# Kernel tuning notes

Hardware: AMD Instinct MI355X
Metric: run time of the kernel (lower is better)

The kernel has to match this reference:

```python
import jax, jax.numpy as jnp
import numpy as np

INPUT_SIZE = 2
HIDDEN = 128
OUTPUT = 2
FUTURE = 50


def setup_inputs() -> dict:
    key = jax.random.key(0)
    ks = jax.random.split(key, 7)
    B, T = 4096, 512
    s = 1.0 / np.sqrt(HIDDEN)
    x = jax.random.normal(ks[0], (B, T, INPUT_SIZE), dtype=jnp.float32)
    W_ih = jax.random.uniform(ks[1], (4 * HIDDEN, INPUT_SIZE), minval=-s, maxval=s, dtype=jnp.float32)
    W_hh = jax.random.uniform(ks[2], (4 * HIDDEN, HIDDEN), minval=-s, maxval=s, dtype=jnp.float32)
    b_ih = jax.random.uniform(ks[3], (4 * HIDDEN,), minval=-s, maxval=s, dtype=jnp.float32)
    b_hh = jax.random.uniform(ks[4], (4 * HIDDEN,), minval=-s, maxval=s, dtype=jnp.float32)
    fc_w = jax.random.uniform(ks[5], (OUTPUT, HIDDEN), minval=-s, maxval=s, dtype=jnp.float32)
    fc_b = jax.random.uniform(ks[6], (OUTPUT,), minval=-s, maxval=s, dtype=jnp.float32)
    return {"x": x, "W_ih": W_ih, "W_hh": W_hh, "b_ih": b_ih, "b_hh": b_hh, "fc_w": fc_w, "fc_b": fc_b}


def reference(x, W_ih, W_hh, b_ih, b_hh, fc_w, fc_b):
    B = x.shape[0]

    def cell(h, c, xt):
        # gates: [B, 4H], PyTorch LSTMCell order i, f, g, o
        gates = xt @ W_ih.T + b_ih + h @ W_hh.T + b_hh
        i, f, g, o = jnp.split(gates, 4, axis=-1)
        c_new = jax.nn.sigmoid(f) * c + jax.nn.sigmoid(i) * jnp.tanh(g)
        h_new = jax.nn.sigmoid(o) * jnp.tanh(c_new)
        return h_new, c_new

    h0 = jnp.zeros((B, HIDDEN), dtype=x.dtype)
    c0 = jnp.zeros((B, HIDDEN), dtype=x.dtype)

    def encode_step(carry, xt):
        h, c = carry
        h, c = cell(h, c, xt)
        return (h, c), None

    (h, c), _ = jax.lax.scan(encode_step, (h0, c0), jnp.swapaxes(x, 0, 1))

    def forecast_step(carry, _):
        h, c = carry
        y = h @ fc_w.T + fc_b  # [B, OUTPUT]
        h, c = cell(h, c, y)
        return (h, c), y

    (_, _), ys = jax.lax.scan(forecast_step, (h, c), None, length=FUTURE)
    # ys: [FUTURE, B, OUTPUT] -> torch.cat(outputs, dim=1) -> [B, FUTURE*OUTPUT]
    return jnp.swapaxes(ys, 0, 1).reshape(B, FUTURE * OUTPUT)
```

## Files before the change

### kernel.cpp

```cpp
#include <hip/hip_runtime.h>

#define HIDDEN 128
#define TSTEPS 512
#define NFUT 50
#define BR 16
#define THREADS 512
#define HPITCH 136

typedef __bf16 bf16x8 __attribute__((ext_vector_type(8)));
typedef float floatx4 __attribute__((ext_vector_type(4)));

union B8 { int4 i; bf16x8 v; };

#if defined(__has_builtin)
#  if __has_builtin(__builtin_amdgcn_exp2f)
#    define EXP2F(x) __builtin_amdgcn_exp2f(x)
#  else
#    define EXP2F(x) exp2f(x)
#  endif
#  if __has_builtin(__builtin_amdgcn_rcpf)
#    define RCPF(x) __builtin_amdgcn_rcpf(x)
#  else
#    define RCPF(x) (1.0f / (x))
#  endif
#else
#  define EXP2F(x) exp2f(x)
#  define RCPF(x) (1.0f / (x))
#endif

#define L2E  1.4426950408889634f
#define L2E2 2.8853900817779268f

__global__ __launch_bounds__(THREADS, 2)
void lstm_forecast_kernel(const float* __restrict__ x,
                          const float* __restrict__ W_ih,
                          const float* __restrict__ W_hh,
                          const float* __restrict__ b_ih,
                          const float* __restrict__ b_hh,
                          const float* __restrict__ fc_w,
                          const float* __restrict__ fc_b,
                          float* __restrict__ out) {
    __shared__ __align__(16) uint2  xa[(TSTEPS + 1) * BR];
    __shared__ __align__(16) __bf16 h_lds[2][BR * HPITCH];
    __shared__ __align__(16) float  fcw_lds[2][HIDDEN];

    const int tid  = threadIdx.x;
    const int wave = tid >> 6;
    const int lane = tid & 63;
    const int quad = lane >> 4;
    const int l15  = lane & 15;
    const int rb   = blockIdx.x * BR;

    if (tid < 256) fcw_lds[tid >> 7][tid & 127] = fc_w[tid];

    {
        const int row = tid & 15;
        for (int tb = tid >> 4; tb < TSTEPS + 1; tb += THREADS >> 4) {
            float2 xv = make_float2(0.f, 0.f);
            if (tb < TSTEPS)
                xv = *(const float2*)&x[(size_t)(rb + row) * (2 * TSTEPS) + tb * 2];
            __bf16 x0h = (__bf16)xv.x, x1h = (__bf16)xv.y;
            __bf16 x0r = (__bf16)(xv.x - (float)x0h);
            __bf16 x1r = (__bf16)(xv.y - (float)x1h);
            uint2 d;
            d.x = (unsigned)__builtin_bit_cast(unsigned short, x0h) |
                  ((unsigned)__builtin_bit_cast(unsigned short, x1h) << 16);
            d.y = (unsigned)__builtin_bit_cast(unsigned short, x0r) |
                  ((unsigned)__builtin_bit_cast(unsigned short, x1r) << 16);
            xa[tb * BR + row] = d;
        }
    }
    for (int i = tid; i < BR * HPITCH; i += THREADS) h_lds[0][i] = (__bf16)0.0f;

    bf16x8 bfrag[4][4];
    B8 bfx[4];
    float wih0[4], wih1[4], bsum[4], gs[4];
    const int u = wave * 16 + l15;
    const float fcb0 = fc_b[0], fcb1 = fc_b[1];
#pragma unroll
    for (int g = 0; g < 4; ++g) {
        gs[g] = (g == 2) ? -L2E2 : -L2E;
        const int cg = g * HIDDEN + u;
        wih0[g] = W_ih[cg * 2 + 0];
        wih1[g] = W_ih[cg * 2 + 1];
        bsum[g] = b_ih[cg] + b_hh[cg];
#pragma unroll
        for (int ks = 0; ks < 4; ++ks) {
            const float* wp = W_hh + (size_t)cg * HIDDEN + ks * 32 + quad * 8;
            bf16x8 bb;
#pragma unroll
            for (int j = 0; j < 8; ++j) bb[j] = (__bf16)(gs[g] * wp[j]);
            bfrag[g][ks] = bb;
        }
        B8 t; t.i = make_int4(0, 0, 0, 0);
        if (quad == 0) {
            const float w0s = gs[g] * wih0[g], w1s = gs[g] * wih1[g], bss = gs[g] * bsum[g];
            __bf16 w0h = (__bf16)w0s, w1h = (__bf16)w1s;
            __bf16 w0l = (__bf16)(w0s - (float)w0h);
            __bf16 w1l = (__bf16)(w1s - (float)w1h);
            __bf16 bh  = (__bf16)bss;
            __bf16 bl  = (__bf16)(bss - (float)bh);
            bf16x8 bv = {w0h, w1h, bh, bl, w0h, w1h, w0l, w1l};
            t.v = bv;
        }
        bfx[g] = t;
    }

    const unsigned ones2 = 0x3F803F80u;

    float cst[4] = {0.f, 0.f, 0.f, 0.f};

    auto ew = [&](floatx4 a0, floatx4 a1, floatx4 a2, floatx4 a3, __bf16* hd) {
        float hn[4];
#pragma unroll
        for (int p = 0; p < 2; ++p) {
            const int r0 = 2 * p, r1 = 2 * p + 1;
            const float ea0 = EXP2F(a0[r0]), ea1 = EXP2F(a0[r1]);
            const float eb0 = EXP2F(a2[r0]), eb1 = EXP2F(a2[r1]);
            const float ec0 = EXP2F(a1[r0]), ec1 = EXP2F(a1[r1]);
            const float A0 = 1.f + ea0, B0 = 1.f + eb0, C0 = 1.f + ec0;
            const float A1v = 1.f + ea1, B1v = 1.f + eb1, C1v = 1.f + ec1;
            const float AB0 = A0 * B0, AB1 = A1v * B1v;
            const float D0 = AB0 * C0, D1 = AB1 * C1v;
            const float I  = RCPF(D0 * D1);
            const float R0 = I * D1, R1 = I * D0;
            const float sf0 = AB0 * R0, sf1 = AB1 * R1;
            const float ig0 = (1.f - eb0) * (C0 * R0);
            const float ig1 = (1.f - eb1) * (C1v * R1);
            const float cn0 = fmaf(sf0, cst[r0], ig0);
            const float cn1 = fmaf(sf1, cst[r1], ig1);
            cst[r0] = cn0; cst[r1] = cn1;
            const float ed0 = EXP2F(fminf(-L2E2 * cn0, 29.f));
            const float ed1 = EXP2F(fminf(-L2E2 * cn1, 29.f));
            const float eo0 = EXP2F(a3[r0]), eo1 = EXP2F(a3[r1]);
            const float E0 = (1.f + ed0) * (1.f + eo0);
            const float E1 = (1.f + ed1) * (1.f + eo1);
            const float J  = RCPF(E0 * E1);
            hn[r0] = (1.f - ed0) * (J * E1);
            hn[r1] = (1.f - ed1) * (J * E0);
        }
#pragma unroll
        for (int r = 0; r < 4; ++r)
            hd[(quad * 4 + r) * HPITCH + u] = (__bf16)hn[r];
    };

    __syncthreads();

    floatx4 acc[4];
    const floatx4 z = {0.f, 0.f, 0.f, 0.f};
    {
        const uint2 xd = xa[0 * BR + l15];
        B8 xf; xf.i = make_int4((int)xd.x, (int)ones2, (int)xd.y, (int)xd.x);
#pragma unroll
        for (int g = 0; g < 4; ++g)
            acc[g] = __builtin_amdgcn_mfma_f32_16x16x32_bf16(xf.v, bfx[g].v, z, 0, 0, 0);
    }

    auto cellE = [&](const __bf16* hs, __bf16* hd, int tn) {
        bf16x8 af[4];
#pragma unroll
        for (int ks = 0; ks < 4; ++ks)
            af[ks] = *(const bf16x8*)&hs[l15 * HPITCH + ks * 32 + quad * 8];
#pragma unroll
        for (int ks = 0; ks < 4; ++ks)
#pragma unroll
            for (int g = 0; g < 4; ++g)
                acc[g] = __builtin_amdgcn_mfma_f32_16x16x32_bf16(af[ks], bfrag[g][ks], acc[g], 0, 0, 0);
        ew(acc[0], acc[1], acc[2], acc[3], hd);
        {
            const uint2 xd = xa[tn * BR + l15];
            B8 xf; xf.i = make_int4((int)xd.x, (int)ones2, (int)xd.y, (int)xd.x);
#pragma unroll
            for (int g = 0; g < 4; ++g)
                acc[g] = __builtin_amdgcn_mfma_f32_16x16x32_bf16(xf.v, bfx[g].v, z, 0, 0, 0);
        }
        __syncthreads();
    };

    for (int t = 0; t < TSTEPS; t += 2) {
        cellE(h_lds[0], h_lds[1], t + 1);
        cellE(h_lds[1], h_lds[0], t + 2);
    }

#pragma unroll
    for (int g = 0; g < 4; ++g) {
        const float bs2 = gs[g] * (bsum[g] + wih0[g] * fcb0 + wih1[g] * fcb1);
#pragma unroll
        for (int ks = 0; ks < 4; ++ks) {
            const int k0 = ks * 32 + quad * 8;
            bf16x8 bb = bfrag[g][ks];
#pragma unroll
            for (int j = 0; j < 8; ++j) {
                const float wv = (float)bb[j] + gs[g] * (wih0[g] * fcw_lds[0][k0 + j]
                                                      + wih1[g] * fcw_lds[1][k0 + j]);
                bb[j] = (__bf16)wv;
            }
            bfrag[g][ks] = bb;
        }
        B8 t; t.i = make_int4(0, 0, 0, 0);
        if (quad == 0) {
            __bf16 bh = (__bf16)bs2;
            __bf16 bl = (__bf16)(bs2 - (float)bh);
            bf16x8 bv = {(__bf16)0.f, (__bf16)0.f, bh, bl,
                         (__bf16)0.f, (__bf16)0.f, (__bf16)0.f, (__bf16)0.f};
            t.v = bv;
        }
        bfx[g] = t;
    }
    B8 xfF; xfF.i = make_int4(0, (int)ones2, 0, 0);

#pragma unroll
    for (int g = 0; g < 4; ++g)
        acc[g] = __builtin_amdgcn_mfma_f32_16x16x32_bf16(xfF.v, bfx[g].v, z, 0, 0, 0);

    auto cellF = [&](const __bf16* hs, __bf16* hd) {
        bf16x8 af[4];
#pragma unroll
        for (int ks = 0; ks < 4; ++ks)
            af[ks] = *(const bf16x8*)&hs[l15 * HPITCH + ks * 32 + quad * 8];
#pragma unroll
        for (int ks = 0; ks < 4; ++ks)
#pragma unroll
            for (int g = 0; g < 4; ++g)
                acc[g] = __builtin_amdgcn_mfma_f32_16x16x32_bf16(af[ks], bfrag[g][ks], acc[g], 0, 0, 0);
        ew(acc[0], acc[1], acc[2], acc[3], hd);
#pragma unroll
        for (int g = 0; g < 4; ++g)
            acc[g] = __builtin_amdgcn_mfma_f32_16x16x32_bf16(xfF.v, bfx[g].v, z, 0, 0, 0);
        __syncthreads();
    };

    auto emitY = [&](const __bf16* hs, int f) {
        if (wave == 0) {
            const int r = lane & 15, seg = lane >> 4;
            const __bf16* hp = &hs[r * HPITCH + seg * 32];
            float p0 = 0.f, p1 = 0.f;
#pragma unroll
            for (int js = 0; js < 4; ++js) {
                bf16x8 hv = *(const bf16x8*)&hp[js * 8];
                const float4* f0 = (const float4*)&fcw_lds[0][seg * 32 + js * 8];
                const float4* f1 = (const float4*)&fcw_lds[1][seg * 32 + js * 8];
                float4 a0 = f0[0], b0 = f0[1], a1 = f1[0], b1 = f1[1];
                p0 += (float)hv[0]*a0.x + (float)hv[1]*a0.y + (float)hv[2]*a0.z + (float)hv[3]*a0.w
                    + (float)hv[4]*b0.x + (float)hv[5]*b0.y + (float)hv[6]*b0.z + (float)hv[7]*b0.w;
                p1 += (float)hv[0]*a1.x + (float)hv[1]*a1.y + (float)hv[2]*a1.z + (float)hv[3]*a1.w
                    + (float)hv[4]*b1.x + (float)hv[5]*b1.y + (float)hv[6]*b1.z + (float)hv[7]*b1.w;
            }
            p0 += __shfl_xor(p0, 16); p0 += __shfl_xor(p0, 32);
            p1 += __shfl_xor(p1, 16); p1 += __shfl_xor(p1, 32);
            if (seg == 0) {
                float* op = &out[(size_t)(rb + r) * (2 * NFUT) + f * 2];
                op[0] = p0 + fcb0;
                op[1] = p1 + fcb1;
            }
        }
    };

    for (int f = 0; f < NFUT; f += 2) {
        emitY(h_lds[0], f);
        cellF(h_lds[0], h_lds[1]);
        emitY(h_lds[1], f + 1);
        cellF(h_lds[1], h_lds[0]);
    }
}

extern "C" void kernel_launch(void* const* d_in, const int* in_sizes, int n_in,
                              void* d_out, int out_size, void* d_ws, size_t ws_size,
                              hipStream_t stream) {
    const float* x    = (const float*)d_in[0];
    const float* W_ih = (const float*)d_in[1];
    const float* W_hh = (const float*)d_in[2];
    const float* b_ih = (const float*)d_in[3];
    const float* b_hh = (const float*)d_in[4];
    const float* fc_w = (const float*)d_in[5];
    const float* fc_b = (const float*)d_in[6];
    float* out = (float*)d_out;

    const int B = in_sizes[0] / (TSTEPS * 2);
    const int grid = B / BR;
    lstm_forecast_kernel<<<grid, THREADS, 0, stream>>>(x, W_ih, W_hh, b_ih, b_hh, fc_w, fc_b, out);
}
```

Before: 542.6 us.

## Split 16-row batch tile into two half-occupied MFMA tiles per step

Each block's 16 batch rows are now spread across two separate 16-row MFMA tiles in which only 8 rows are live. The remaining rows are masked to zero by an input mask and are otherwise discarded. This doubles the MFMA work per step but halves the elementwise gate work per lane, from 4 rows to 2, and gives two independent accumulator chains that can interleave. The x-projection MFMA also moves from the end of the previous step into the current step. The change adds LDS space and register pressure, and the MFMA-issue portion of each step becomes longer.

```diff
diff --git a/kernel.cpp b/kernel.cpp
--- a/kernel.cpp
+++ b/kernel.cpp
@@ -40,8 +40,8 @@
                           const float* __restrict__ fc_w,
                           const float* __restrict__ fc_b,
                           float* __restrict__ out) {
-    __shared__ __align__(16) uint2  xa[(TSTEPS + 1) * BR];
-    __shared__ __align__(16) __bf16 h_lds[2][BR * HPITCH];
+    __shared__ __align__(16) uint2  xa[TSTEPS * BR];
+    __shared__ __align__(16) __bf16 hb[2][2][16 * HPITCH];
     __shared__ __align__(16) float  fcw_lds[2][HIDDEN];
 
     const int tid  = threadIdx.x;
@@ -55,10 +55,8 @@
 
     {
         const int row = tid & 15;
-        for (int tb = tid >> 4; tb < TSTEPS + 1; tb += THREADS >> 4) {
-            float2 xv = make_float2(0.f, 0.f);
-            if (tb < TSTEPS)
-                xv = *(const float2*)&x[(size_t)(rb + row) * (2 * TSTEPS) + tb * 2];
+        for (int tb = tid >> 4; tb < TSTEPS; tb += THREADS >> 4) {
+            float2 xv = *(const float2*)&x[(size_t)(rb + row) * (2 * TSTEPS) + tb * 2];
             __bf16 x0h = (__bf16)xv.x, x1h = (__bf16)xv.y;
             __bf16 x0r = (__bf16)(xv.x - (float)x0h);
             __bf16 x1r = (__bf16)(xv.y - (float)x1h);
@@ -70,7 +68,8 @@
             xa[tb * BR + row] = d;
         }
     }
-    for (int i = tid; i < BR * HPITCH; i += THREADS) h_lds[0][i] = (__bf16)0.0f;
+    for (int i = tid; i < 2 * 2 * 16 * HPITCH; i += THREADS)
+        ((__bf16*)hb)[i] = (__bf16)0.0f;
 
     bf16x8 bfrag[4][4];
     B8 bfx[4];
@@ -108,78 +107,82 @@
 
     const unsigned ones2 = 0x3F803F80u;
 
-    float cst[4] = {0.f, 0.f, 0.f, 0.f};
-
-    auto ew = [&](floatx4 a0, floatx4 a1, floatx4 a2, floatx4 a3, __bf16* hd) {
-        float hn[4];
-#pragma unroll
-        for (int p = 0; p < 2; ++p) {
-            const int r0 = 2 * p, r1 = 2 * p + 1;
-            const float ea0 = EXP2F(a0[r0]), ea1 = EXP2F(a0[r1]);
-            const float eb0 = EXP2F(a2[r0]), eb1 = EXP2F(a2[r1]);
-            const float ec0 = EXP2F(a1[r0]), ec1 = EXP2F(a1[r1]);
-            const float A0 = 1.f + ea0, B0 = 1.f + eb0, C0 = 1.f + ec0;
-            const float A1v = 1.f + ea1, B1v = 1.f + eb1, C1v = 1.f + ec1;
-            const float AB0 = A0 * B0, AB1 = A1v * B1v;
-            const float D0 = AB0 * C0, D1 = AB1 * C1v;
-            const float I  = RCPF(D0 * D1);
-            const float R0 = I * D1, R1 = I * D0;
-            const float sf0 = AB0 * R0, sf1 = AB1 * R1;
-            const float ig0 = (1.f - eb0) * (C0 * R0);
-            const float ig1 = (1.f - eb1) * (C1v * R1);
-            const float cn0 = fmaf(sf0, cst[r0], ig0);
-            const float cn1 = fmaf(sf1, cst[r1], ig1);
-            cst[r0] = cn0; cst[r1] = cn1;
-            const float ed0 = EXP2F(fminf(-L2E2 * cn0, 29.f));
-            const float ed1 = EXP2F(fminf(-L2E2 * cn1, 29.f));
-            const float eo0 = EXP2F(a3[r0]), eo1 = EXP2F(a3[r1]);
-            const float E0 = (1.f + ed0) * (1.f + eo0);
-            const float E1 = (1.f + ed1) * (1.f + eo1);
-            const float J  = RCPF(E0 * E1);
-            hn[r0] = (1.f - ed0) * (J * E1);
-            hn[r1] = (1.f - ed1) * (J * E0);
-        }
-#pragma unroll
-        for (int r = 0; r < 4; ++r)
-            hd[(quad * 4 + r) * HPITCH + u] = (__bf16)hn[r];
+    float cst0[2] = {0.f, 0.f};
+    float cst1[2] = {0.f, 0.f};
+
+    const int xr = ((l15 >> 2) << 1) + (l15 & 1);
+    const unsigned rm = ((l15 & 2) == 0) ? 0xFFFFFFFFu : 0u;
+
+    auto ewg = [&](floatx4 A0, floatx4 A1, floatx4 A2, floatx4 A3,
+                   float* cs, __bf16* hd) {
+        const float ea0 = EXP2F(A0[0]), ea1 = EXP2F(A0[1]);
+        const float eb0 = EXP2F(A2[0]), eb1 = EXP2F(A2[1]);
+        const float ec0 = EXP2F(A1[0]), ec1 = EXP2F(A1[1]);
+        const float a0v = 1.f + ea0, b0v = 1.f + eb0, c0v = 1.f + ec0;
+        const float a1v = 1.f + ea1, b1v = 1.f + eb1, c1v = 1.f + ec1;
+        const float AB0 = a0v * b0v, AB1 = a1v * b1v;
+        const float D0 = AB0 * c0v, D1 = AB1 * c1v;
+        const float I  = RCPF(D0 * D1);
+        const float R0 = I * D1, R1 = I * D0;
+        const float sf0 = AB0 * R0, sf1 = AB1 * R1;
+        const float ig0 = (1.f - eb0) * (c0v * R0);
+        const float ig1 = (1.f - eb1) * (c1v * R1);
+        const float cn0 = fmaf(sf0, cs[0], ig0);
+        const float cn1 = fmaf(sf1, cs[1], ig1);
+        cs[0] = cn0; cs[1] = cn1;
+        const float ed0 = EXP2F(fminf(-L2E2 * cn0, 29.f));
+        const float ed1 = EXP2F(fminf(-L2E2 * cn1, 29.f));
+        const float eo0 = EXP2F(A3[0]), eo1 = EXP2F(A3[1]);
+        const float E0 = (1.f + ed0) * (1.f + eo0);
+        const float E1 = (1.f + ed1) * (1.f + eo1);
+        const float J  = RCPF(E0 * E1);
+        const float hn0 = (1.f - ed0) * (J * E1);
+        const float hn1 = (1.f - ed1) * (J * E0);
+        hd[(quad * 4 + 0) * HPITCH + u] = (__bf16)hn0;
+        hd[(quad * 4 + 1) * HPITCH + u] = (__bf16)hn1;
+    };
+
+    const floatx4 z = {0.f, 0.f, 0.f, 0.f};
+
+    auto cellE = [&](int sb, int t) {
+        const int db = sb ^ 1;
+        bf16x8 af0[4], af1[4];
+#pragma unroll
+        for (int ks = 0; ks < 4; ++ks) {
+            af0[ks] = *(const bf16x8*)&hb[sb][0][l15 * HPITCH + ks * 32 + quad * 8];
+            af1[ks] = *(const bf16x8*)&hb[sb][1][l15 * HPITCH + ks * 32 + quad * 8];
+        }
+        const uint2 xd0 = xa[t * BR + xr];
+        const uint2 xd1 = xa[t * BR + 8 + xr];
+        B8 xf0; xf0.i = make_int4((int)(xd0.x & rm), (int)(ones2 & rm), (int)(xd0.y & rm), (int)(xd0.x & rm));
+        B8 xf1; xf1.i = make_int4((int)(xd1.x & rm), (int)(ones2 & rm), (int)(xd1.y & rm), (int)(xd1.x & rm));
+        floatx4 acc0[4], acc1[4];
+#pragma unroll
+        for (int g = 0; g < 4; ++g)
+            acc0[g] = __builtin_amdgcn_mfma_f32_16x16x32_bf16(xf0.v, bfx[g].v, z, 0, 0, 0);
+#pragma unroll
+        for (int ks = 0; ks < 4; ++ks)
+#pragma unroll
+            for (int g = 0; g < 4; ++g)
+                acc0[g] = __builtin_amdgcn_mfma_f32_16x16x32_bf16(af0[ks], bfrag[g][ks], acc0[g], 0, 0, 0);
+#pragma unroll
+        for (int g = 0; g < 4; ++g)
+            acc1[g] = __builtin_amdgcn_mfma_f32_16x16x32_bf16(xf1.v, bfx[g].v, z, 0, 0, 0);
+#pragma unroll
+        for (int ks = 0; ks < 4; ++ks)
+#pragma unroll
+            for (int g = 0; g < 4; ++g)
+                acc1[g] = __builtin_amdgcn_mfma_f32_16x16x32_bf16(af1[ks], bfrag[g][ks], acc1[g], 0, 0, 0);
+        ewg(acc0[0], acc0[1], acc0[2], acc0[3], cst0, &hb[db][0][0]);
+        ewg(acc1[0], acc1[1], acc1[2], acc1[3], cst1, &hb[db][1][0]);
+        __syncthreads();
     };
 
     __syncthreads();
 
-    floatx4 acc[4];
-    const floatx4 z = {0.f, 0.f, 0.f, 0.f};
-    {
-        const uint2 xd = xa[0 * BR + l15];
-        B8 xf; xf.i = make_int4((int)xd.x, (int)ones2, (int)xd.y, (int)xd.x);
-#pragma unroll
-        for (int g = 0; g < 4; ++g)
-            acc[g] = __builtin_amdgcn_mfma_f32_16x16x32_bf16(xf.v, bfx[g].v, z, 0, 0, 0);
-    }
-
-    auto cellE = [&](const __bf16* hs, __bf16* hd, int tn) {
-        bf16x8 af[4];
-#pragma unroll
-        for (int ks = 0; ks < 4; ++ks)
-            af[ks] = *(const bf16x8*)&hs[l15 * HPITCH + ks * 32 + quad * 8];
-#pragma unroll
-        for (int ks = 0; ks < 4; ++ks)
-#pragma unroll
-            for (int g = 0; g < 4; ++g)
-                acc[g] = __builtin_amdgcn_mfma_f32_16x16x32_bf16(af[ks], bfrag[g][ks], acc[g], 0, 0, 0);
-        ew(acc[0], acc[1], acc[2], acc[3], hd);
-        {
-            const uint2 xd = xa[tn * BR + l15];
-            B8 xf; xf.i = make_int4((int)xd.x, (int)ones2, (int)xd.y, (int)xd.x);
-#pragma unroll
-            for (int g = 0; g < 4; ++g)
-                acc[g] = __builtin_amdgcn_mfma_f32_16x16x32_bf16(xf.v, bfx[g].v, z, 0, 0, 0);
-        }
-        __syncthreads();
-    };
-
     for (int t = 0; t < TSTEPS; t += 2) {
-        cellE(h_lds[0], h_lds[1], t + 1);
-        cellE(h_lds[1], h_lds[0], t + 2);
+        cellE(0, t);
+        cellE(1, t + 1);
     }
 
 #pragma unroll
@@ -209,31 +212,42 @@
     }
     B8 xfF; xfF.i = make_int4(0, (int)ones2, 0, 0);
 
-#pragma unroll
-    for (int g = 0; g < 4; ++g)
-        acc[g] = __builtin_amdgcn_mfma_f32_16x16x32_bf16(xfF.v, bfx[g].v, z, 0, 0, 0);
-
-    auto cellF = [&](const __bf16* hs, __bf16* hd) {
-        bf16x8 af[4];
-#pragma unroll
-        for (int ks = 0; ks < 4; ++ks)
-            af[ks] = *(const bf16x8*)&hs[l15 * HPITCH + ks * 32 + quad * 8];
-#pragma unroll
-        for (int ks = 0; ks < 4; ++ks)
-#pragma unroll
-            for (int g = 0; g < 4; ++g)
-                acc[g] = __builtin_amdgcn_mfma_f32_16x16x32_bf16(af[ks], bfrag[g][ks], acc[g], 0, 0, 0);
-        ew(acc[0], acc[1], acc[2], acc[3], hd);
-#pragma unroll
-        for (int g = 0; g < 4; ++g)
-            acc[g] = __builtin_amdgcn_mfma_f32_16x16x32_bf16(xfF.v, bfx[g].v, z, 0, 0, 0);
+    auto cellF = [&](int sb) {
+        const int db = sb ^ 1;
+        bf16x8 af0[4], af1[4];
+#pragma unroll
+        for (int ks = 0; ks < 4; ++ks) {
+            af0[ks] = *(const bf16x8*)&hb[sb][0][l15 * HPITCH + ks * 32 + quad * 8];
+            af1[ks] = *(const bf16x8*)&hb[sb][1][l15 * HPITCH + ks * 32 + quad * 8];
+        }
+        floatx4 acc0[4], acc1[4];
+#pragma unroll
+        for (int g = 0; g < 4; ++g)
+            acc0[g] = __builtin_amdgcn_mfma_f32_16x16x32_bf16(xfF.v, bfx[g].v, z, 0, 0, 0);
+#pragma unroll
+        for (int ks = 0; ks < 4; ++ks)
+#pragma unroll
+            for (int g = 0; g < 4; ++g)
+                acc0[g] = __builtin_amdgcn_mfma_f32_16x16x32_bf16(af0[ks], bfrag[g][ks], acc0[g], 0, 0, 0);
+#pragma unroll
+        for (int g = 0; g < 4; ++g)
+            acc1[g] = __builtin_amdgcn_mfma_f32_16x16x32_bf16(xfF.v, bfx[g].v, z, 0, 0, 0);
+#pragma unroll
+        for (int ks = 0; ks < 4; ++ks)
+#pragma unroll
+            for (int g = 0; g < 4; ++g)
+                acc1[g] = __builtin_amdgcn_mfma_f32_16x16x32_bf16(af1[ks], bfrag[g][ks], acc1[g], 0, 0, 0);
+        ewg(acc0[0], acc0[1], acc0[2], acc0[3], cst0, &hb[db][0][0]);
+        ewg(acc1[0], acc1[1], acc1[2], acc1[3], cst1, &hb[db][1][0]);
         __syncthreads();
     };
 
-    auto emitY = [&](const __bf16* hs, int f) {
+    auto emitY = [&](int sb, int f) {
         if (wave == 0) {
             const int r = lane & 15, seg = lane >> 4;
-            const __bf16* hp = &hs[r * HPITCH + seg * 32];
+            const int g = r >> 3, rr = r & 7;
+            const int slot = ((rr >> 1) << 2) + (rr & 1);
+            const __bf16* hp = &hb[sb][g][slot * HPITCH + seg * 32];
             float p0 = 0.f, p1 = 0.f;
 #pragma unroll
             for (int js = 0; js < 4; ++js) {
@@ -257,10 +271,10 @@
     };
 
     for (int f = 0; f < NFUT; f += 2) {
-        emitY(h_lds[0], f);
-        cellF(h_lds[0], h_lds[1]);
-        emitY(h_lds[1], f + 1);
-        cellF(h_lds[1], h_lds[0]);
+        emitY(0, f);
+        cellF(0);
+        emitY(1, f + 1);
+        cellF(1);
     }
 }
 
```

Result: slower. 670.2 us (+23.5%).

## Halve block to 4 waves, each computing two 16-unit hidden column chunks

Applied to the files above, without the earlier changes.

The block shrinks from 8 to 4 waves, and each wave now owns two 16-column hidden chunks, so twice the W_hh fragments sit in registers per thread. The x-projection MFMA moves from the tail of the previous step to the start of each cell. This cuts barrier participants and raises per-wave MFMA work, giving more independent MFMA chains to interleave with the elementwise math. The cost is higher register pressure (launch bounds relaxed to one block per EU setting) and possibly lower occupancy. The x-input MFMA is also no longer overlapped across the barrier.

```diff
diff --git a/kernel.cpp b/kernel.cpp
--- a/kernel.cpp
+++ b/kernel.cpp
@@ -4,7 +4,7 @@
 #define TSTEPS 512
 #define NFUT 50
 #define BR 16
-#define THREADS 512
+#define THREADS 256
 #define HPITCH 136
 
 typedef __bf16 bf16x8 __attribute__((ext_vector_type(8)));
@@ -31,7 +31,7 @@
 #define L2E  1.4426950408889634f
 #define L2E2 2.8853900817779268f
 
-__global__ __launch_bounds__(THREADS, 2)
+__global__ __launch_bounds__(THREADS, 1)
 void lstm_forecast_kernel(const float* __restrict__ x,
                           const float* __restrict__ W_ih,
                           const float* __restrict__ W_hh,
@@ -51,7 +51,7 @@
     const int l15  = lane & 15;
     const int rb   = blockIdx.x * BR;
 
-    if (tid < 256) fcw_lds[tid >> 7][tid & 127] = fc_w[tid];
+    fcw_lds[tid >> 7][tid & 127] = fc_w[tid];
 
     {
         const int row = tid & 15;
@@ -72,52 +72,58 @@
     }
     for (int i = tid; i < BR * HPITCH; i += THREADS) h_lds[0][i] = (__bf16)0.0f;
 
-    bf16x8 bfrag[4][4];
-    B8 bfx[4];
-    float wih0[4], wih1[4], bsum[4], gs[4];
-    const int u = wave * 16 + l15;
+    bf16x8 bfrag[2][4][4];
+    B8 bfx[2][4];
+    float wih0[2][4], wih1[2][4], bsum[2][4], gs[4];
+    int u[2];
+    u[0] = wave * 32 + l15;
+    u[1] = u[0] + 16;
     const float fcb0 = fc_b[0], fcb1 = fc_b[1];
 #pragma unroll
-    for (int g = 0; g < 4; ++g) {
-        gs[g] = (g == 2) ? -L2E2 : -L2E;
-        const int cg = g * HIDDEN + u;
-        wih0[g] = W_ih[cg * 2 + 0];
-        wih1[g] = W_ih[cg * 2 + 1];
-        bsum[g] = b_ih[cg] + b_hh[cg];
-#pragma unroll
-        for (int ks = 0; ks < 4; ++ks) {
-            const float* wp = W_hh + (size_t)cg * HIDDEN + ks * 32 + quad * 8;
-            bf16x8 bb;
-#pragma unroll
-            for (int j = 0; j < 8; ++j) bb[j] = (__bf16)(gs[g] * wp[j]);
-            bfrag[g][ks] = bb;
-        }
-        B8 t; t.i = make_int4(0, 0, 0, 0);
-        if (quad == 0) {
-            const float w0s = gs[g] * wih0[g], w1s = gs[g] * wih1[g], bss = gs[g] * bsum[g];
-            __bf16 w0h = (__bf16)w0s, w1h = (__bf16)w1s;
-            __bf16 w0l = (__bf16)(w0s - (float)w0h);
-            __bf16 w1l = (__bf16)(w1s - (float)w1h);
-            __bf16 bh  = (__bf16)bss;
-            __bf16 bl  = (__bf16)(bss - (float)bh);
-            bf16x8 bv = {w0h, w1h, bh, bl, w0h, w1h, w0l, w1l};
-            t.v = bv;
-        }
-        bfx[g] = t;
+    for (int ch = 0; ch < 2; ++ch) {
+#pragma unroll
+        for (int g = 0; g < 4; ++g) {
+            gs[g] = (g == 2) ? -L2E2 : -L2E;
+            const int cg = g * HIDDEN + u[ch];
+            wih0[ch][g] = W_ih[cg * 2 + 0];
+            wih1[ch][g] = W_ih[cg * 2 + 1];
+            bsum[ch][g] = b_ih[cg] + b_hh[cg];
+#pragma unroll
+            for (int ks = 0; ks < 4; ++ks) {
+                const float* wp = W_hh + (size_t)cg * HIDDEN + ks * 32 + quad * 8;
+                bf16x8 bb;
+#pragma unroll
+                for (int j = 0; j < 8; ++j) bb[j] = (__bf16)(gs[g] * wp[j]);
+                bfrag[ch][g][ks] = bb;
+            }
+            B8 t; t.i = make_int4(0, 0, 0, 0);
+            if (quad == 0) {
+                const float w0s = gs[g] * wih0[ch][g], w1s = gs[g] * wih1[ch][g];
+                const float bss = gs[g] * bsum[ch][g];
+                __bf16 w0h = (__bf16)w0s, w1h = (__bf16)w1s;
+                __bf16 w0l = (__bf16)(w0s - (float)w0h);
+                __bf16 w1l = (__bf16)(w1s - (float)w1h);
+                __bf16 bh  = (__bf16)bss;
+                __bf16 bl  = (__bf16)(bss - (float)bh);
+                bf16x8 bv = {w0h, w1h, bh, bl, w0h, w1h, w0l, w1l};
+                t.v = bv;
+            }
+            bfx[ch][g] = t;
+        }
     }
 
     const unsigned ones2 = 0x3F803F80u;
 
-    float cst[4] = {0.f, 0.f, 0.f, 0.f};
-
-    auto ew = [&](floatx4 a0, floatx4 a1, floatx4 a2, floatx4 a3, __bf16* hd) {
+    float cst[2][4] = {{0.f, 0.f, 0.f, 0.f}, {0.f, 0.f, 0.f, 0.f}};
+
+    auto ew = [&](const floatx4* a, float* cs, int uc, __bf16* hd) {
         float hn[4];
 #pragma unroll
         for (int p = 0; p < 2; ++p) {
             const int r0 = 2 * p, r1 = 2 * p + 1;
-            const float ea0 = EXP2F(a0[r0]), ea1 = EXP2F(a0[r1]);
-            const float eb0 = EXP2F(a2[r0]), eb1 = EXP2F(a2[r1]);
-            const float ec0 = EXP2F(a1[r0]), ec1 = EXP2F(a1[r1]);
+            const float ea0 = EXP2F(a[0][r0]), ea1 = EXP2F(a[0][r1]);
+            const float eb0 = EXP2F(a[2][r0]), eb1 = EXP2F(a[2][r1]);
+            const float ec0 = EXP2F(a[1][r0]), ec1 = EXP2F(a[1][r1]);
             const float A0 = 1.f + ea0, B0 = 1.f + eb0, C0 = 1.f + ec0;
             const float A1v = 1.f + ea1, B1v = 1.f + eb1, C1v = 1.f + ec1;
             const float AB0 = A0 * B0, AB1 = A1v * B1v;
@@ -127,12 +133,12 @@
             const float sf0 = AB0 * R0, sf1 = AB1 * R1;
             const float ig0 = (1.f - eb0) * (C0 * R0);
             const float ig1 = (1.f - eb1) * (C1v * R1);
-            const float cn0 = fmaf(sf0, cst[r0], ig0);
-            const float cn1 = fmaf(sf1, cst[r1], ig1);
-            cst[r0] = cn0; cst[r1] = cn1;
+            const float cn0 = fmaf(sf0, cs[r0], ig0);
+            const float cn1 = fmaf(sf1, cs[r1], ig1);
+            cs[r0] = cn0; cs[r1] = cn1;
             const float ed0 = EXP2F(fminf(-L2E2 * cn0, 29.f));
             const float ed1 = EXP2F(fminf(-L2E2 * cn1, 29.f));
-            const float eo0 = EXP2F(a3[r0]), eo1 = EXP2F(a3[r1]);
+            const float eo0 = EXP2F(a[3][r0]), eo1 = EXP2F(a[3][r1]);
             const float E0 = (1.f + ed0) * (1.f + eo0);
             const float E1 = (1.f + ed1) * (1.f + eo1);
             const float J  = RCPF(E0 * E1);
@@ -141,92 +147,93 @@
         }
 #pragma unroll
         for (int r = 0; r < 4; ++r)
-            hd[(quad * 4 + r) * HPITCH + u] = (__bf16)hn[r];
+            hd[(quad * 4 + r) * HPITCH + uc] = (__bf16)hn[r];
+    };
+
+    const floatx4 z = {0.f, 0.f, 0.f, 0.f};
+
+    auto cellE = [&](const __bf16* hs, __bf16* hd, int t) {
+        bf16x8 af[4];
+#pragma unroll
+        for (int ks = 0; ks < 4; ++ks)
+            af[ks] = *(const bf16x8*)&hs[l15 * HPITCH + ks * 32 + quad * 8];
+        const uint2 xd = xa[t * BR + l15];
+        B8 xf; xf.i = make_int4((int)xd.x, (int)ones2, (int)xd.y, (int)xd.x);
+        floatx4 acc[2][4];
+#pragma unroll
+        for (int ch = 0; ch < 2; ++ch)
+#pragma unroll
+            for (int g = 0; g < 4; ++g)
+                acc[ch][g] = __builtin_amdgcn_mfma_f32_16x16x32_bf16(xf.v, bfx[ch][g].v, z, 0, 0, 0);
+#pragma unroll
+        for (int ks = 0; ks < 4; ++ks)
+#pragma unroll
+            for (int ch = 0; ch < 2; ++ch)
+#pragma unroll
+                for (int g = 0; g < 4; ++g)
+                    acc[ch][g] = __builtin_amdgcn_mfma_f32_16x16x32_bf16(af[ks], bfrag[ch][g][ks], acc[ch][g], 0, 0, 0);
+        ew(acc[0], cst[0], u[0], hd);
+        ew(acc[1], cst[1], u[1], hd);
+        __syncthreads();
     };
 
     __syncthreads();
 
-    floatx4 acc[4];
-    const floatx4 z = {0.f, 0.f, 0.f, 0.f};
-    {
-        const uint2 xd = xa[0 * BR + l15];
-        B8 xf; xf.i = make_int4((int)xd.x, (int)ones2, (int)xd.y, (int)xd.x);
-#pragma unroll
-        for (int g = 0; g < 4; ++g)
-            acc[g] = __builtin_amdgcn_mfma_f32_16x16x32_bf16(xf.v, bfx[g].v, z, 0, 0, 0);
-    }
-
-    auto cellE = [&](const __bf16* hs, __bf16* hd, int tn) {
-        bf16x8 af[4];
-#pragma unroll
-        for (int ks = 0; ks < 4; ++ks)
-            af[ks] = *(const bf16x8*)&hs[l15 * HPITCH + ks * 32 + quad * 8];
-#pragma unroll
-        for (int ks = 0; ks < 4; ++ks)
-#pragma unroll
-            for (int g = 0; g < 4; ++g)
-                acc[g] = __builtin_amdgcn_mfma_f32_16x16x32_bf16(af[ks], bfrag[g][ks], acc[g], 0, 0, 0);
-        ew(acc[0], acc[1], acc[2], acc[3], hd);
-        {
-            const uint2 xd = xa[tn * BR + l15];
-            B8 xf; xf.i = make_int4((int)xd.x, (int)ones2, (int)xd.y, (int)xd.x);
-#pragma unroll
-            for (int g = 0; g < 4; ++g)
-                acc[g] = __builtin_amdgcn_mfma_f32_16x16x32_bf16(xf.v, bfx[g].v, z, 0, 0, 0);
-        }
-        __syncthreads();
-    };
-
     for (int t = 0; t < TSTEPS; t += 2) {
-        cellE(h_lds[0], h_lds[1], t + 1);
-        cellE(h_lds[1], h_lds[0], t + 2);
-    }
-
-#pragma unroll
-    for (int g = 0; g < 4; ++g) {
-        const float bs2 = gs[g] * (bsum[g] + wih0[g] * fcb0 + wih1[g] * fcb1);
-#pragma unroll
-        for (int ks = 0; ks < 4; ++ks) {
-            const int k0 = ks * 32 + quad * 8;
-            bf16x8 bb = bfrag[g][ks];
-#pragma unroll
-            for (int j = 0; j < 8; ++j) {
-                const float wv = (float)bb[j] + gs[g] * (wih0[g] * fcw_lds[0][k0 + j]
-                                                      + wih1[g] * fcw_lds[1][k0 + j]);
-                bb[j] = (__bf16)wv;
-            }
-            bfrag[g][ks] = bb;
-        }
-        B8 t; t.i = make_int4(0, 0, 0, 0);
-        if (quad == 0) {
-            __bf16 bh = (__bf16)bs2;
-            __bf16 bl = (__bf16)(bs2 - (float)bh);
-            bf16x8 bv = {(__bf16)0.f, (__bf16)0.f, bh, bl,
-                         (__bf16)0.f, (__bf16)0.f, (__bf16)0.f, (__bf16)0.f};
-            t.v = bv;
-        }
-        bfx[g] = t;
+        cellE(h_lds[0], h_lds[1], t);
+        cellE(h_lds[1], h_lds[0], t + 1);
+    }
+
+#pragma unroll
+    for (int ch = 0; ch < 2; ++ch) {
+#pragma unroll
+        for (int g = 0; g < 4; ++g) {
+            const float bs2 = gs[g] * (bsum[ch][g] + wih0[ch][g] * fcb0 + wih1[ch][g] * fcb1);
+#pragma unroll
+            for (int ks = 0; ks < 4; ++ks) {
+                const int k0 = ks * 32 + quad * 8;
+                bf16x8 bb = bfrag[ch][g][ks];
+#pragma unroll
+                for (int j = 0; j < 8; ++j) {
+                    const float wv = (float)bb[j] + gs[g] * (wih0[ch][g] * fcw_lds[0][k0 + j]
+                                                          + wih1[ch][g] * fcw_lds[1][k0 + j]);
+                    bb[j] = (__bf16)wv;
+                }
+                bfrag[ch][g][ks] = bb;
+            }
+            B8 t; t.i = make_int4(0, 0, 0, 0);
+            if (quad == 0) {
+                __bf16 bh = (__bf16)bs2;
+                __bf16 bl = (__bf16)(bs2 - (float)bh);
+                bf16x8 bv = {(__bf16)0.f, (__bf16)0.f, bh, bl,
+                             (__bf16)0.f, (__bf16)0.f, (__bf16)0.f, (__bf16)0.f};
+                t.v = bv;
+            }
+            bfx[ch][g] = t;
+        }
     }
     B8 xfF; xfF.i = make_int4(0, (int)ones2, 0, 0);
-
-#pragma unroll
-    for (int g = 0; g < 4; ++g)
-        acc[g] = __builtin_amdgcn_mfma_f32_16x16x32_bf16(xfF.v, bfx[g].v, z, 0, 0, 0);
 
     auto cellF = [&](const __bf16* hs, __bf16* hd) {
         bf16x8 af[4];
 #pragma unroll
         for (int ks = 0; ks < 4; ++ks)
             af[ks] = *(const bf16x8*)&hs[l15 * HPITCH + ks * 32 + quad * 8];
-#pragma unroll
-        for (int ks = 0; ks < 4; ++ks)
+        floatx4 acc[2][4];
+#pragma unroll
+        for (int ch = 0; ch < 2; ++ch)
 #pragma unroll
             for (int g = 0; g < 4; ++g)
-                acc[g] = __builtin_amdgcn_mfma_f32_16x16x32_bf16(af[ks], bfrag[g][ks], acc[g], 0, 0, 0);
-        ew(acc[0], acc[1], acc[2], acc[3], hd);
-#pragma unroll
-        for (int g = 0; g < 4; ++g)
-            acc[g] = __builtin_amdgcn_mfma_f32_16x16x32_bf16(xfF.v, bfx[g].v, z, 0, 0, 0);
+                acc[ch][g] = __builtin_amdgcn_mfma_f32_16x16x32_bf16(xfF.v, bfx[ch][g].v, z, 0, 0, 0);
+#pragma unroll
+        for (int ks = 0; ks < 4; ++ks)
+#pragma unroll
+            for (int ch = 0; ch < 2; ++ch)
+#pragma unroll
+                for (int g = 0; g < 4; ++g)
+                    acc[ch][g] = __builtin_amdgcn_mfma_f32_16x16x32_bf16(af[ks], bfrag[ch][g][ks], acc[ch][g], 0, 0, 0);
+        ew(acc[0], cst[0], u[0], hd);
+        ew(acc[1], cst[1], u[1], hd);
         __syncthreads();
     };
 
```

New measurement: 610.6 us. 12.5% more time.
